# Kernel optimization log

Measured on AMD Instinct MI355X. Metric: run time of the kernel, lower is better.

The kernel has to match this reference:

```python
import jax, jax.numpy as jnp
import numpy as np

N = 4096
D = 256
H = 8
HD = D // H
EPS = 1e-5
NEG = -1e9


def layer_norm(x, g, b):
    mu = jnp.mean(x, axis=-1, keepdims=True)
    var = jnp.mean(jnp.square(x - mu), axis=-1, keepdims=True)
    return (x - mu) * jax.lax.rsqrt(var + EPS) * g + b


def setup_inputs() -> dict:
    key = jax.random.key(0)
    ks = jax.random.split(key, 12)
    s = 1.0 / np.sqrt(D)
    inp = {
        "x": jax.random.normal(ks[0], (N, D), dtype=jnp.float32),
        "adj": jax.random.randint(ks[1], (N, N), 0, 2, dtype=jnp.int32),
        "Wq": jax.random.uniform(ks[2], (D, D), jnp.float32, -s, s),
        "Wk": jax.random.uniform(ks[3], (D, D), jnp.float32, -s, s),
        "Wv": jax.random.uniform(ks[4], (D, D), jnp.float32, -s, s),
        "bq": jnp.zeros((D,), jnp.float32),
        "bk": jnp.zeros((D,), jnp.float32),
        "bv": jnp.zeros((D,), jnp.float32),
        "Wo": jax.random.uniform(ks[5], (D, D), jnp.float32, -s, s),
        "bo": jnp.zeros((D,), jnp.float32),
        "g1": jnp.ones((D,), jnp.float32),
        "beta1": jnp.zeros((D,), jnp.float32),
        "W1": jax.random.uniform(ks[6], (2 * D, D), jnp.float32, -s, s),
        "b1": jnp.zeros((2 * D,), jnp.float32),
        "W2": jax.random.uniform(ks[7], (D, 2 * D), jnp.float32, -1.0 / np.sqrt(2 * D), 1.0 / np.sqrt(2 * D)),
        "b2": jnp.zeros((D,), jnp.float32),
        "g2": jnp.ones((D,), jnp.float32),
        "beta2": jnp.zeros((D,), jnp.float32),
    }
    return inp


def reference(x, adj, Wq, Wk, Wv, bq, bk, bv, Wo, bo, g1, beta1, W1, b1, W2, b2, g2, beta2):
    n = adj.shape[0]
    # allowed = adj + I > 0 ; attention only over neighbors + self-loop
    allowed = (adj + jnp.eye(n, dtype=adj.dtype)) > 0  # (n, n) bool

    q = (x @ Wq.T + bq).reshape(n, H, HD)
    k = (x @ Wk.T + bk).reshape(n, H, HD)
    v = (x @ Wv.T + bv).reshape(n, H, HD)

    scale = 1.0 / np.sqrt(HD)
    scores = jnp.einsum('nhd,mhd->hnm', q, k) * scale  # (H, n, n)
    scores = jnp.where(allowed[None, :, :], scores, NEG)
    attn = jax.nn.softmax(scores, axis=-1)
    o = jnp.einsum('hnm,mhd->nhd', attn, v).reshape(n, D)
    h = o @ Wo.T + bo

    x = layer_norm(x + h, g1, beta1)
    ffn = jax.nn.relu(x @ W1.T + b1) @ W2.T + b2
    x = layer_norm(x + ffn, g2, beta2)
    return x
```

## Files before the change

kernel.cpp:

```cpp
#include <hip/hip_runtime.h>
#include <hip/hip_bf16.h>

typedef __attribute__((ext_vector_type(4))) float f32x4;
typedef __attribute__((ext_vector_type(8))) short s16x8;

#define NROWS 4096
#define DMODEL 256
#define NHEAD 8
#define HDIM 32
#define PSTRIDE 72
#define OSTRIDE 33
#define M2C 24.0f
#define NM (NROWS * DMODEL)
#define SH_S 268
#define SY_S 264
#define SR_S 520

__device__ __forceinline__ short bf16r(float f) {
    union { float f; unsigned u; } v; v.f = f;
    unsigned r = v.u + 0x7fffu + ((v.u >> 16) & 1u);
    return (short)(r >> 16);
}

__device__ __forceinline__ float fexp2(float x) {
    float r;
    asm("v_exp_f32 %0, %1" : "=v"(r) : "v"(x));
    return r;
}

__device__ __forceinline__ unsigned pk_bf16(float a, float b) {
#if __has_builtin(__builtin_amdgcn_cvt_pk_bf16_f32)
    typedef __bf16 bf2 __attribute__((ext_vector_type(2)));
    union { bf2 h; unsigned u; } c;
    c.h = __builtin_amdgcn_cvt_pk_bf16_f32(a, b);
    return c.u;
#else
    return (unsigned)(unsigned short)bf16r(a) | ((unsigned)(unsigned short)bf16r(b) << 16);
#endif
}

__device__ __forceinline__ s16x8 pack8(float4 a, float4 b) {
    s16x8 r;
    r[0] = bf16r(a.x); r[1] = bf16r(a.y); r[2] = bf16r(a.z); r[3] = bf16r(a.w);
    r[4] = bf16r(b.x); r[5] = bf16r(b.y); r[6] = bf16r(b.z); r[7] = bf16r(b.w);
    return r;
}

__global__ __launch_bounds__(256) void qkvprep_kernel(
        const float* __restrict__ X,
        const float* __restrict__ Wq, const float* __restrict__ Wk,
        const float* __restrict__ Wv,
        const float* __restrict__ bq, const float* __restrict__ bk,
        const float* __restrict__ bv,
        const int* __restrict__ adj, unsigned* __restrict__ mask,
        const float* __restrict__ Wo, const float* __restrict__ W1,
        const float* __restrict__ W2, short* __restrict__ Wb,
        short* __restrict__ Qb, short* __restrict__ Kb,
        short* __restrict__ Vswz) {
    __shared__ short sT[64 * 72];
    const int b = blockIdx.x;
    const int tid = threadIdx.x;
    const int lane = tid & 63;
    if (b < 768) {
        const int wv = tid >> 6;
        const int quad = lane >> 4, col = lane & 15;
        const int bx = b & 63, by = b >> 6;
        const int o0 = by * 64;
        const int z = o0 >> 8;
        const float* Wsrc = (z == 0) ? Wq : (z == 1 ? Wk : Wv);
        const float* bias = (z == 0) ? bq : (z == 1 ? bk : bv);
        const int ow0 = o0 & 255;
        const int n0 = bx * 64 + wv * 16;
        const float QSC = 0.25505653437397888f;

        f32x4 zero = {0.f, 0.f, 0.f, 0.f};
        f32x4 acc[4] = {zero, zero, zero, zero};
        const float* ap = X + (size_t)(n0 + col) * DMODEL + quad * 8;
#pragma unroll
        for (int k0 = 0; k0 < DMODEL; k0 += 32) {
            float4 a0 = *(const float4*)(ap + k0);
            float4 a1 = *(const float4*)(ap + k0 + 4);
            s16x8 af = pack8(a0, a1);
#pragma unroll
            for (int t = 0; t < 4; ++t) {
                const float* wp = Wsrc + (size_t)(ow0 + t * 16 + col) * DMODEL + quad * 8 + k0;
                s16x8 bf = pack8(*(const float4*)wp, *(const float4*)(wp + 4));
                acc[t] = __builtin_amdgcn_mfma_f32_16x16x32_bf16(af, bf, acc[t], 0, 0, 0);
            }
        }
        if (z != 2) {
#pragma unroll
            for (int t = 0; t < 4; ++t) {
                const int oo = ow0 + t * 16 + col;
                float bvv = bias[oo];
#pragma unroll
                for (int r = 0; r < 4; ++r) {
                    int n = n0 + quad * 4 + r;
                    float v = acc[t][r] + bvv;
                    if (z == 0) Qb[(size_t)n * DMODEL + oo] = bf16r(v * QSC);
                    else        Kb[(size_t)(oo >> 5) * NROWS * HDIM + (size_t)n * HDIM + (oo & 31)] = bf16r(v);
                }
            }
        } else {
#pragma unroll
            for (int t = 0; t < 4; ++t) {
                const int oot = t * 16 + col;
                float bvv = bias[ow0 + oot];
#pragma unroll
                for (int r = 0; r < 4; ++r) {
                    int nn = wv * 16 + quad * 4 + r;
                    sT[oot * 72 + nn] = bf16r(acc[t][r] + bvv);
                }
            }
            __syncthreads();
            const int f = tid >> 5;
            const int lh = f >> 2, hdh = (f >> 1) & 1, kh = f & 1;
            const int L0 = (tid & 31) * 2;
            const int hgl = (ow0 >> 5) + lh;
            short* dst = Vswz + (((size_t)(hgl * 64 + bx) * 4 + hdh * 2 + kh) * 512);
#pragma unroll
            for (int e = 0; e < 2; ++e) {
                int L = L0 + e;
                int hd_local = lh * 32 + hdh * 16 + (L & 15);
                int key_local = kh * 32 + ((L >> 4) * 8);
                s16x8 v = *(const s16x8*)&sT[hd_local * 72 + key_local];
                *(s16x8*)(dst + L * 8) = v;
            }
        }
    } else if (b < 2816) {
        const int waveid = (b - 768) * 4 + (tid >> 6);
        int4 av[8];
        int rows[8], segs[8];
#pragma unroll
        for (int i = 0; i < 8; ++i) {
            const int task = waveid + i * 8192;
            rows[i] = task >> 4; segs[i] = task & 15;
            av[i] = *(const int4*)(adj + (size_t)rows[i] * NROWS + segs[i] * 256 + lane * 4);
        }
#pragma unroll
        for (int i = 0; i < 8; ++i) {
            const int row = rows[i];
            const int c0 = segs[i] * 256 + lane * 4;
            unsigned nib = (unsigned)(av[i].x > 0 || c0 == row)
                         | ((unsigned)(av[i].y > 0 || c0 + 1 == row) << 1)
                         | ((unsigned)(av[i].z > 0 || c0 + 2 == row) << 2)
                         | ((unsigned)(av[i].w > 0 || c0 + 3 == row) << 3);
            unsigned v = nib << ((lane & 7) * 4);
            v |= __shfl_xor((int)v, 1, 64);
            v |= __shfl_xor((int)v, 2, 64);
            v |= __shfl_xor((int)v, 4, 64);
            if ((lane & 7) == 0)
                mask[row * 128 + segs[i] * 8 + (lane >> 3)] = v;
        }
    } else {
        int i = (b - 2816) * 2048 + tid * 8;
        const float* src; int off;
        if (i < 65536)       { src = Wo; off = i; }
        else if (i < 196608) { src = W1; off = i - 65536; }
        else                 { src = W2; off = i - 196608; }
        float4 a = *(const float4*)(src + off);
        float4 c = *(const float4*)(src + off + 4);
        *(s16x8*)(Wb + i) = pack8(a, c);
    }
}

__global__ __launch_bounds__(256) void attn_kernel(const short* __restrict__ Qb,
                                                   const short* __restrict__ Kb,
                                                   const short* __restrict__ Vswz,
                                                   const unsigned* __restrict__ mask,
                                                   short* __restrict__ Om) {
    __shared__ union {
        short sP[2][16 * PSTRIDE];
        float sO[HDIM][OSTRIDE];
    } u[4];
    __shared__ float sl[4][32];

    const int tid = threadIdx.x;
    const int wv = tid >> 6, lane = tid & 63;
    const int quad = lane >> 4, col = lane & 15;
    const int h = blockIdx.x & 7;
    const int q0 = (blockIdx.x >> 3) * 32;
    const int kw = wv * 1024;

    s16x8 qf[2];
    qf[0] = *(const s16x8*)(Qb + (size_t)(q0 + col) * DMODEL + h * HDIM + quad * 8);
    qf[1] = *(const s16x8*)(Qb + (size_t)(q0 + 16 + col) * DMODEL + h * HDIM + quad * 8);

    const short* kp = Kb + (size_t)h * NROWS * HDIM + (size_t)(kw + col) * HDIM + quad * 8;
    const short* vbase = Vswz + ((size_t)(h * 64 + (kw >> 6)) * 4) * 512 + lane * 8;
    const unsigned* mp0 = mask + (size_t)(q0 + col) * 128 + (kw >> 5);
    const unsigned* mp1 = mp0 + 16 * 128;

    const short onev = (col == 0) ? (short)0x3F80 : (short)0;
    const s16x8 ones = {onev, onev, onev, onev, onev, onev, onev, onev};

    f32x4 zero = {0.f, 0.f, 0.f, 0.f};
    f32x4 acc[2][2] = {{zero, zero}, {zero, zero}};
    f32x4 lacc[2] = {zero, zero};
    const f32x4 cinit = {-M2C, -M2C, -M2C, -M2C};

#pragma unroll 2
    for (int it = 0; it < 16; ++it) {
        const short* k = kp + it * 64 * HDIM;
        s16x8 kf0 = *(const s16x8*)(k);
        s16x8 kf1 = *(const s16x8*)(k + 16 * HDIM);
        s16x8 kf2 = *(const s16x8*)(k + 32 * HDIM);
        s16x8 kf3 = *(const s16x8*)(k + 48 * HDIM);
        uint2 w0 = *(const uint2*)(mp0 + it * 2);
        uint2 w1 = *(const uint2*)(mp1 + it * 2);
        const short* vb = vbase + it * 4 * 512;
        s16x8 vf00 = *(const s16x8*)(vb);
        s16x8 vf01 = *(const s16x8*)(vb + 512);
        s16x8 vf10 = *(const s16x8*)(vb + 1024);
        s16x8 vf11 = *(const s16x8*)(vb + 1536);

#pragma unroll
        for (int qs = 0; qs < 2; ++qs) {
            unsigned wlo = (qs ? w1.x : w0.x) >> (quad * 4);
            unsigned whi = (qs ? w1.y : w0.y) >> (quad * 4);
            f32x4 st[4];
            st[0] = __builtin_amdgcn_mfma_f32_16x16x32_bf16(kf0, qf[qs], cinit, 0, 0, 0);
            st[1] = __builtin_amdgcn_mfma_f32_16x16x32_bf16(kf1, qf[qs], cinit, 0, 0, 0);
            st[2] = __builtin_amdgcn_mfma_f32_16x16x32_bf16(kf2, qf[qs], cinit, 0, 0, 0);
            st[3] = __builtin_amdgcn_mfma_f32_16x16x32_bf16(kf3, qf[qs], cinit, 0, 0, 0);

            float p[4][4];
#pragma unroll
            for (int t = 0; t < 4; ++t) {
                unsigned wm = (t < 2) ? wlo : whi;
#pragma unroll
                for (int r = 0; r < 4; ++r) {
                    float e = fexp2(st[t][r]);
                    bool ok = (wm & (1u << ((t & 1) * 16 + r))) != 0u;
                    p[t][r] = ok ? e : 0.f;
                }
            }

            short* pb = &u[wv].sP[qs][0];
#pragma unroll
            for (int t = 0; t < 4; ++t) {
                uint2 pr;
                pr.x = pk_bf16(p[t][0], p[t][1]);
                pr.y = pk_bf16(p[t][2], p[t][3]);
                *(uint2*)(pb + col * PSTRIDE + t * 16 + quad * 4) = pr;
            }
            s16x8 pb0 = *(const s16x8*)(pb + col * PSTRIDE + quad * 8);
            s16x8 pb1 = *(const s16x8*)(pb + col * PSTRIDE + 32 + quad * 8);

            acc[qs][0] = __builtin_amdgcn_mfma_f32_16x16x32_bf16(vf00, pb0, acc[qs][0], 0, 0, 0);
            acc[qs][0] = __builtin_amdgcn_mfma_f32_16x16x32_bf16(vf01, pb1, acc[qs][0], 0, 0, 0);
            acc[qs][1] = __builtin_amdgcn_mfma_f32_16x16x32_bf16(vf10, pb0, acc[qs][1], 0, 0, 0);
            acc[qs][1] = __builtin_amdgcn_mfma_f32_16x16x32_bf16(vf11, pb1, acc[qs][1], 0, 0, 0);
            lacc[qs] = __builtin_amdgcn_mfma_f32_16x16x32_bf16(ones, pb0, lacc[qs], 0, 0, 0);
            lacc[qs] = __builtin_amdgcn_mfma_f32_16x16x32_bf16(ones, pb1, lacc[qs], 0, 0, 0);
        }
    }

#pragma unroll
    for (int qs = 0; qs < 2; ++qs) {
        if (lane < 16) sl[wv][qs * 16 + col] = lacc[qs][0];
#pragma unroll
        for (int rr = 0; rr < 4; ++rr) {
            u[wv].sO[quad * 4 + rr][qs * 16 + col]      = acc[qs][0][rr];
            u[wv].sO[16 + quad * 4 + rr][qs * 16 + col] = acc[qs][1][rr];
        }
    }
    __syncthreads();

    const int q = tid >> 3, hd0 = (tid & 7) * 4;
    float l = sl[0][q] + sl[1][q] + sl[2][q] + sl[3][q];
    float inv = 1.f / l;
    float4 ov;
    ov.x = u[0].sO[hd0][q]     + u[1].sO[hd0][q]     + u[2].sO[hd0][q]     + u[3].sO[hd0][q];
    ov.y = u[0].sO[hd0 + 1][q] + u[1].sO[hd0 + 1][q] + u[2].sO[hd0 + 1][q] + u[3].sO[hd0 + 1][q];
    ov.z = u[0].sO[hd0 + 2][q] + u[1].sO[hd0 + 2][q] + u[2].sO[hd0 + 2][q] + u[3].sO[hd0 + 2][q];
    ov.w = u[0].sO[hd0 + 3][q] + u[1].sO[hd0 + 3][q] + u[2].sO[hd0 + 3][q] + u[3].sO[hd0 + 3][q];
    uint2 ob;
    ob.x = pk_bf16(ov.x * inv, ov.y * inv);
    ob.y = pk_bf16(ov.z * inv, ov.w * inv);
    *(uint2*)(Om + (size_t)(q0 + q) * DMODEL + h * HDIM + hd0) = ob;
}

__global__ __launch_bounds__(512) void mega_kernel(
        const short* __restrict__ Omb,
        const float* __restrict__ X,
        const short* __restrict__ Wob, const short* __restrict__ W1b,
        const short* __restrict__ W2b,
        const float* __restrict__ bo,
        const float* __restrict__ g1, const float* __restrict__ be1,
        const float* __restrict__ b1, const float* __restrict__ b2,
        const float* __restrict__ g2, const float* __restrict__ be2,
        float* __restrict__ out) {
    __shared__ short sR[16 * SR_S];
    __shared__ float sH[16 * SH_S];
    __shared__ short sY[16 * SY_S];

    const int tid = threadIdx.x;
    const int wv = tid >> 6, lane = tid & 63;
    const int quad = lane >> 4, col = lane & 15;
    const int n0 = blockIdx.x * 16;
    const int rr_ = tid >> 5, c8 = (tid & 31) * 8;
    const int n_ln = n0 + rr_;
    f32x4 zero = {0.f, 0.f, 0.f, 0.f};

    {
        const int o0 = wv * 32;
        f32x4 acc[2] = {zero, zero};
#pragma unroll
        for (int k0 = 0; k0 < DMODEL; k0 += 32) {
            s16x8 af = *(const s16x8*)(Omb + (size_t)(n0 + col) * DMODEL + k0 + quad * 8);
#pragma unroll
            for (int t = 0; t < 2; ++t) {
                s16x8 bf = *(const s16x8*)(Wob + (size_t)(o0 + t * 16 + col) * DMODEL + k0 + quad * 8);
                acc[t] = __builtin_amdgcn_mfma_f32_16x16x32_bf16(af, bf, acc[t], 0, 0, 0);
            }
        }
#pragma unroll
        for (int t = 0; t < 2; ++t) {
            int o = o0 + t * 16 + col;
            float bv = bo[o];
#pragma unroll
            for (int r = 0; r < 4; ++r)
                sH[(quad * 4 + r) * SH_S + o] = acc[t][r] + bv;
        }
    }
    __syncthreads();

    float y1v[8];
    {
        const float* xp = X + (size_t)n_ln * DMODEL + c8;
        float v[8];
        float s = 0.f;
#pragma unroll
        for (int j = 0; j < 2; ++j) {
            float4 xv = ((const float4*)xp)[j];
            float4 hv = *(const float4*)&sH[rr_ * SH_S + c8 + j * 4];
            v[j * 4 + 0] = xv.x + hv.x; v[j * 4 + 1] = xv.y + hv.y;
            v[j * 4 + 2] = xv.z + hv.z; v[j * 4 + 3] = xv.w + hv.w;
            s += v[j * 4] + v[j * 4 + 1] + v[j * 4 + 2] + v[j * 4 + 3];
        }
#pragma unroll
        for (int m = 1; m < 32; m <<= 1) s += __shfl_xor(s, m, 64);
        float mean = s * (1.f / 256.f);
        float q = 0.f;
#pragma unroll
        for (int i = 0; i < 8; ++i) { v[i] -= mean; q += v[i] * v[i]; }
#pragma unroll
        for (int m = 1; m < 32; m <<= 1) q += __shfl_xor(q, m, 64);
        float rstd = rsqrtf(q * (1.f / 256.f) + 1e-5f);
        const float* gp = g1 + c8;
        const float* bp = be1 + c8;
        s16x8 w;
#pragma unroll
        for (int j = 0; j < 2; ++j) {
            float4 gv = ((const float4*)gp)[j];
            float4 bev = ((const float4*)bp)[j];
            float a0 = v[j * 4 + 0] * rstd * gv.x + bev.x;
            float a1 = v[j * 4 + 1] * rstd * gv.y + bev.y;
            float a2 = v[j * 4 + 2] * rstd * gv.z + bev.z;
            float a3 = v[j * 4 + 3] * rstd * gv.w + bev.w;
            y1v[j * 4 + 0] = a0; y1v[j * 4 + 1] = a1;
            y1v[j * 4 + 2] = a2; y1v[j * 4 + 3] = a3;
            *((unsigned*)&w + j * 2 + 0) = pk_bf16(a0, a1);
            *((unsigned*)&w + j * 2 + 1) = pk_bf16(a2, a3);
        }
        *(s16x8*)&sY[rr_ * SY_S + c8] = w;
    }
    __syncthreads();

    {
        const int o0 = wv * 64;
        f32x4 acc[4] = {zero, zero, zero, zero};
#pragma unroll
        for (int k0 = 0; k0 < DMODEL; k0 += 32) {
            s16x8 af = *(const s16x8*)&sY[col * SY_S + k0 + quad * 8];
#pragma unroll
            for (int t = 0; t < 4; ++t) {
                s16x8 bf = *(const s16x8*)(W1b + (size_t)(o0 + t * 16 + col) * DMODEL + k0 + quad * 8);
                acc[t] = __builtin_amdgcn_mfma_f32_16x16x32_bf16(af, bf, acc[t], 0, 0, 0);
            }
        }
#pragma unroll
        for (int t = 0; t < 4; ++t) {
            int o = o0 + t * 16 + col;
            float bv = b1[o];
#pragma unroll
            for (int r = 0; r < 4; ++r)
                sR[(quad * 4 + r) * SR_S + o] = bf16r(fmaxf(acc[t][r] + bv, 0.f));
        }
    }
    __syncthreads();

    {
        const int o0 = wv * 32;
        f32x4 acc[2] = {zero, zero};
#pragma unroll
        for (int k0 = 0; k0 < 512; k0 += 32) {
            s16x8 af = *(const s16x8*)&sR[col * SR_S + k0 + quad * 8];
#pragma unroll
            for (int t = 0; t < 2; ++t) {
                s16x8 bf = *(const s16x8*)(W2b + (size_t)(o0 + t * 16 + col) * 512 + k0 + quad * 8);
                acc[t] = __builtin_amdgcn_mfma_f32_16x16x32_bf16(af, bf, acc[t], 0, 0, 0);
            }
        }
#pragma unroll
        for (int t = 0; t < 2; ++t) {
            int o = o0 + t * 16 + col;
            float bv = b2[o];
#pragma unroll
            for (int r = 0; r < 4; ++r)
                sH[(quad * 4 + r) * SH_S + o] = acc[t][r] + bv;
        }
    }
    __syncthreads();

    {
        float v[8];
        float s = 0.f;
#pragma unroll
        for (int j = 0; j < 2; ++j) {
            float4 hv = *(const float4*)&sH[rr_ * SH_S + c8 + j * 4];
            v[j * 4 + 0] = y1v[j * 4 + 0] + hv.x; v[j * 4 + 1] = y1v[j * 4 + 1] + hv.y;
            v[j * 4 + 2] = y1v[j * 4 + 2] + hv.z; v[j * 4 + 3] = y1v[j * 4 + 3] + hv.w;
            s += v[j * 4] + v[j * 4 + 1] + v[j * 4 + 2] + v[j * 4 + 3];
        }
#pragma unroll
        for (int m = 1; m < 32; m <<= 1) s += __shfl_xor(s, m, 64);
        float mean = s * (1.f / 256.f);
        float q = 0.f;
#pragma unroll
        for (int i = 0; i < 8; ++i) { v[i] -= mean; q += v[i] * v[i]; }
#pragma unroll
        for (int m = 1; m < 32; m <<= 1) q += __shfl_xor(q, m, 64);
        float rstd = rsqrtf(q * (1.f / 256.f) + 1e-5f);
        const float* gp = g2 + c8;
        const float* bp = be2 + c8;
        float* op = out + (size_t)n_ln * DMODEL + c8;
#pragma unroll
        for (int j = 0; j < 2; ++j) {
            float4 gv = ((const float4*)gp)[j];
            float4 bev = ((const float4*)bp)[j];
            float4 y;
            y.x = v[j * 4 + 0] * rstd * gv.x + bev.x;
            y.y = v[j * 4 + 1] * rstd * gv.y + bev.y;
            y.z = v[j * 4 + 2] * rstd * gv.z + bev.z;
            y.w = v[j * 4 + 3] * rstd * gv.w + bev.w;
            ((float4*)op)[j] = y;
        }
    }
}

extern "C" void kernel_launch(void* const* d_in, const int* in_sizes, int n_in,
                              void* d_out, int out_size, void* d_ws, size_t ws_size,
                              hipStream_t stream) {
    const float* x   = (const float*)d_in[0];
    const int*   adj = (const int*)d_in[1];
    const float* Wq  = (const float*)d_in[2];
    const float* Wk  = (const float*)d_in[3];
    const float* Wv  = (const float*)d_in[4];
    const float* bq  = (const float*)d_in[5];
    const float* bk  = (const float*)d_in[6];
    const float* bv  = (const float*)d_in[7];
    const float* Wo  = (const float*)d_in[8];
    const float* bo  = (const float*)d_in[9];
    const float* g1  = (const float*)d_in[10];
    const float* be1 = (const float*)d_in[11];
    const float* W1  = (const float*)d_in[12];
    const float* b1  = (const float*)d_in[13];
    const float* W2  = (const float*)d_in[14];
    const float* b2  = (const float*)d_in[15];
    const float* g2  = (const float*)d_in[16];
    const float* be2 = (const float*)d_in[17];
    float* out = (float*)d_out;

    char* p = (char*)d_ws;
    unsigned* mask = (unsigned*)p; p += (size_t)NROWS * 128 * 4;
    short* Wb   = (short*)p;       p += (size_t)327680 * 2;
    short* Qb   = (short*)p;       p += (size_t)NM * 2;
    short* Kb   = (short*)p;       p += (size_t)NM * 2;
    short* Vswz = (short*)p;       p += (size_t)NM * 2;
    short* Omb  = (short*)p;       p += (size_t)NM * 2;

    qkvprep_kernel<<<dim3(2976), dim3(256), 0, stream>>>(
        x, Wq, Wk, Wv, bq, bk, bv, adj, mask, Wo, W1, W2, Wb, Qb, Kb, Vswz);
    attn_kernel<<<dim3(1024), dim3(256), 0, stream>>>(Qb, Kb, Vswz, mask, Omb);
    mega_kernel<<<dim3(256), dim3(512), 0, stream>>>(
        Omb, x, Wb, Wb + 65536, Wb + 196608,
        bo, g1, be1, b1, b2, g2, be2, out);
}
```

Measured before the change: 224.8 us.

## Pre-convert X and QKV weights to bf16 in a separate kernel; LUT-based mask in attention

The fused prep kernel is split in two. The first kernel builds the adjacency bitmask and converts Wo/W1/W2, Wq/Wk/Wv and X to bf16. The second runs the QKV projection from those bf16 buffers, so the GEMM no longer repacks fp32 to bf16 on every load. The attention inner loop now applies the mask by ANDing packed bf16 exp values with 16-bit masks fetched from a small shared-memory lookup table, replacing the per-element select. The split adds a kernel launch and an extra global round trip for X, and the table adds LDS reads per tile.

```diff
diff --git a/kernel.cpp b/kernel.cpp
--- a/kernel.cpp
+++ b/kernel.cpp
@@ -46,89 +46,18 @@
     return r;
 }
 
-__global__ __launch_bounds__(256) void qkvprep_kernel(
-        const float* __restrict__ X,
-        const float* __restrict__ Wq, const float* __restrict__ Wk,
-        const float* __restrict__ Wv,
-        const float* __restrict__ bq, const float* __restrict__ bk,
-        const float* __restrict__ bv,
+__global__ __launch_bounds__(256) void prep1_kernel(
         const int* __restrict__ adj, unsigned* __restrict__ mask,
         const float* __restrict__ Wo, const float* __restrict__ W1,
         const float* __restrict__ W2, short* __restrict__ Wb,
-        short* __restrict__ Qb, short* __restrict__ Kb,
-        short* __restrict__ Vswz) {
-    __shared__ short sT[64 * 72];
+        const float* __restrict__ Wq, const float* __restrict__ Wk,
+        const float* __restrict__ Wv, short* __restrict__ Wqkvb,
+        const float* __restrict__ X, short* __restrict__ Xb) {
     const int b = blockIdx.x;
     const int tid = threadIdx.x;
     const int lane = tid & 63;
-    if (b < 768) {
-        const int wv = tid >> 6;
-        const int quad = lane >> 4, col = lane & 15;
-        const int bx = b & 63, by = b >> 6;
-        const int o0 = by * 64;
-        const int z = o0 >> 8;
-        const float* Wsrc = (z == 0) ? Wq : (z == 1 ? Wk : Wv);
-        const float* bias = (z == 0) ? bq : (z == 1 ? bk : bv);
-        const int ow0 = o0 & 255;
-        const int n0 = bx * 64 + wv * 16;
-        const float QSC = 0.25505653437397888f;
-
-        f32x4 zero = {0.f, 0.f, 0.f, 0.f};
-        f32x4 acc[4] = {zero, zero, zero, zero};
-        const float* ap = X + (size_t)(n0 + col) * DMODEL + quad * 8;
-#pragma unroll
-        for (int k0 = 0; k0 < DMODEL; k0 += 32) {
-            float4 a0 = *(const float4*)(ap + k0);
-            float4 a1 = *(const float4*)(ap + k0 + 4);
-            s16x8 af = pack8(a0, a1);
-#pragma unroll
-            for (int t = 0; t < 4; ++t) {
-                const float* wp = Wsrc + (size_t)(ow0 + t * 16 + col) * DMODEL + quad * 8 + k0;
-                s16x8 bf = pack8(*(const float4*)wp, *(const float4*)(wp + 4));
-                acc[t] = __builtin_amdgcn_mfma_f32_16x16x32_bf16(af, bf, acc[t], 0, 0, 0);
-            }
-        }
-        if (z != 2) {
-#pragma unroll
-            for (int t = 0; t < 4; ++t) {
-                const int oo = ow0 + t * 16 + col;
-                float bvv = bias[oo];
-#pragma unroll
-                for (int r = 0; r < 4; ++r) {
-                    int n = n0 + quad * 4 + r;
-                    float v = acc[t][r] + bvv;
-                    if (z == 0) Qb[(size_t)n * DMODEL + oo] = bf16r(v * QSC);
-                    else        Kb[(size_t)(oo >> 5) * NROWS * HDIM + (size_t)n * HDIM + (oo & 31)] = bf16r(v);
-                }
-            }
-        } else {
-#pragma unroll
-            for (int t = 0; t < 4; ++t) {
-                const int oot = t * 16 + col;
-                float bvv = bias[ow0 + oot];
-#pragma unroll
-                for (int r = 0; r < 4; ++r) {
-                    int nn = wv * 16 + quad * 4 + r;
-                    sT[oot * 72 + nn] = bf16r(acc[t][r] + bvv);
-                }
-            }
-            __syncthreads();
-            const int f = tid >> 5;
-            const int lh = f >> 2, hdh = (f >> 1) & 1, kh = f & 1;
-            const int L0 = (tid & 31) * 2;
-            const int hgl = (ow0 >> 5) + lh;
-            short* dst = Vswz + (((size_t)(hgl * 64 + bx) * 4 + hdh * 2 + kh) * 512);
-#pragma unroll
-            for (int e = 0; e < 2; ++e) {
-                int L = L0 + e;
-                int hd_local = lh * 32 + hdh * 16 + (L & 15);
-                int key_local = kh * 32 + ((L >> 4) * 8);
-                s16x8 v = *(const s16x8*)&sT[hd_local * 72 + key_local];
-                *(s16x8*)(dst + L * 8) = v;
-            }
-        }
-    } else if (b < 2816) {
-        const int waveid = (b - 768) * 4 + (tid >> 6);
+    if (b < 2048) {
+        const int waveid = b * 4 + (tid >> 6);
         int4 av[8];
         int rows[8], segs[8];
 #pragma unroll
@@ -152,15 +81,96 @@
             if ((lane & 7) == 0)
                 mask[row * 128 + segs[i] * 8 + (lane >> 3)] = v;
         }
-    } else {
-        int i = (b - 2816) * 2048 + tid * 8;
+    } else if (b < 2208) {
+        int i = (b - 2048) * 2048 + tid * 8;
         const float* src; int off;
         if (i < 65536)       { src = Wo; off = i; }
         else if (i < 196608) { src = W1; off = i - 65536; }
         else                 { src = W2; off = i - 196608; }
-        float4 a = *(const float4*)(src + off);
-        float4 c = *(const float4*)(src + off + 4);
-        *(s16x8*)(Wb + i) = pack8(a, c);
+        *(s16x8*)(Wb + i) = pack8(*(const float4*)(src + off), *(const float4*)(src + off + 4));
+    } else if (b < 2304) {
+        int i = (b - 2208) * 2048 + tid * 8;
+        const float* src; int off;
+        if (i < 65536)       { src = Wq; off = i; }
+        else if (i < 131072) { src = Wk; off = i - 65536; }
+        else                 { src = Wv; off = i - 131072; }
+        *(s16x8*)(Wqkvb + i) = pack8(*(const float4*)(src + off), *(const float4*)(src + off + 4));
+    } else {
+        int i = (b - 2304) * 2048 + tid * 8;
+        *(s16x8*)(Xb + i) = pack8(*(const float4*)(X + i), *(const float4*)(X + i + 4));
+    }
+}
+
+__global__ __launch_bounds__(256) void prep2_kernel(
+        const short* __restrict__ Xb, const short* __restrict__ Wqkvb,
+        const float* __restrict__ bq, const float* __restrict__ bk,
+        const float* __restrict__ bv,
+        short* __restrict__ Qb, short* __restrict__ Kb,
+        short* __restrict__ Vswz) {
+    __shared__ short sT[64 * 72];
+    const int b = blockIdx.x;
+    const int tid = threadIdx.x;
+    const int lane = tid & 63;
+    const int wv = tid >> 6;
+    const int quad = lane >> 4, col = lane & 15;
+    const int bx = b & 63, by = b >> 6;
+    const int o0 = by * 64;
+    const int z = o0 >> 8;
+    const float* bias = (z == 0) ? bq : (z == 1 ? bk : bv);
+    const int ow0 = o0 & 255;
+    const int n0 = bx * 64 + wv * 16;
+    const float QSC = 0.25505653437397888f;
+
+    f32x4 zero = {0.f, 0.f, 0.f, 0.f};
+    f32x4 acc[4] = {zero, zero, zero, zero};
+    const short* ap = Xb + (size_t)(n0 + col) * DMODEL + quad * 8;
+#pragma unroll
+    for (int k0 = 0; k0 < DMODEL; k0 += 32) {
+        s16x8 af = *(const s16x8*)(ap + k0);
+#pragma unroll
+        for (int t = 0; t < 4; ++t) {
+            s16x8 bf = *(const s16x8*)(Wqkvb + (size_t)(o0 + t * 16 + col) * DMODEL + quad * 8 + k0);
+            acc[t] = __builtin_amdgcn_mfma_f32_16x16x32_bf16(af, bf, acc[t], 0, 0, 0);
+        }
+    }
+    if (z != 2) {
+#pragma unroll
+        for (int t = 0; t < 4; ++t) {
+            const int oo = ow0 + t * 16 + col;
+            float bvv = bias[oo];
+#pragma unroll
+            for (int r = 0; r < 4; ++r) {
+                int n = n0 + quad * 4 + r;
+                float v = acc[t][r] + bvv;
+                if (z == 0) Qb[(size_t)n * DMODEL + oo] = bf16r(v * QSC);
+                else        Kb[(size_t)(oo >> 5) * NROWS * HDIM + (size_t)n * HDIM + (oo & 31)] = bf16r(v);
+            }
+        }
+    } else {
+#pragma unroll
+        for (int t = 0; t < 4; ++t) {
+            const int oot = t * 16 + col;
+            float bvv = bias[ow0 + oot];
+#pragma unroll
+            for (int r = 0; r < 4; ++r) {
+                int nn = wv * 16 + quad * 4 + r;
+                sT[oot * 72 + nn] = bf16r(acc[t][r] + bvv);
+            }
+        }
+        __syncthreads();
+        const int f = tid >> 5;
+        const int lh = f >> 2, hdh = (f >> 1) & 1, kh = f & 1;
+        const int L0 = (tid & 31) * 2;
+        const int hgl = (ow0 >> 5) + lh;
+        short* dst = Vswz + (((size_t)(hgl * 64 + bx) * 4 + hdh * 2 + kh) * 512);
+#pragma unroll
+        for (int e = 0; e < 2; ++e) {
+            int L = L0 + e;
+            int hd_local = lh * 32 + hdh * 16 + (L & 15);
+            int key_local = kh * 32 + ((L >> 4) * 8);
+            s16x8 v = *(const s16x8*)&sT[hd_local * 72 + key_local];
+            *(s16x8*)(dst + L * 8) = v;
+        }
     }
 }
 
@@ -174,6 +184,7 @@
         float sO[HDIM][OSTRIDE];
     } u[4];
     __shared__ float sl[4][32];
+    __shared__ __align__(16) unsigned lut2[32];
 
     const int tid = threadIdx.x;
     const int wv = tid >> 6, lane = tid & 63;
@@ -182,6 +193,14 @@
     const int q0 = (blockIdx.x >> 3) * 32;
     const int kw = wv * 1024;
 
+    if (tid < 32) {
+        int i = tid >> 1;
+        unsigned b0 = (tid & 1) ? ((i >> 2) & 1u) : (i & 1u);
+        unsigned b1 = (tid & 1) ? ((i >> 3) & 1u) : ((i >> 1) & 1u);
+        lut2[tid] = (b0 ? 0xFFFFu : 0u) | (b1 ? 0xFFFF0000u : 0u);
+    }
+    __syncthreads();
+
     s16x8 qf[2];
     qf[0] = *(const s16x8*)(Qb + (size_t)(q0 + col) * DMODEL + h * HDIM + quad * 8);
     qf[1] = *(const s16x8*)(Qb + (size_t)(q0 + 16 + col) * DMODEL + h * HDIM + quad * 8);
@@ -198,6 +217,8 @@
     f32x4 acc[2][2] = {{zero, zero}, {zero, zero}};
     f32x4 lacc[2] = {zero, zero};
     const f32x4 cinit = {-M2C, -M2C, -M2C, -M2C};
+    const int sh_lo = quad * 4, sh_hi = 16 + quad * 4;
+    const char* lb = (const char*)lut2;
 
 #pragma unroll 2
     for (int it = 0; it < 16; ++it) {
@@ -216,34 +237,34 @@
 
 #pragma unroll
         for (int qs = 0; qs < 2; ++qs) {
-            unsigned wlo = (qs ? w1.x : w0.x) >> (quad * 4);
-            unsigned whi = (qs ? w1.y : w0.y) >> (quad * 4);
+            const unsigned wx = qs ? w1.x : w0.x;
+            const unsigned wy = qs ? w1.y : w0.y;
+            uint2 m0 = *(const uint2*)(lb + (((wx >> sh_lo) & 0xF) << 3));
+            uint2 m1 = *(const uint2*)(lb + (((wx >> sh_hi) & 0xF) << 3));
+            uint2 m2 = *(const uint2*)(lb + (((wy >> sh_lo) & 0xF) << 3));
+            uint2 m3 = *(const uint2*)(lb + (((wy >> sh_hi) & 0xF) << 3));
+
             f32x4 st[4];
             st[0] = __builtin_amdgcn_mfma_f32_16x16x32_bf16(kf0, qf[qs], cinit, 0, 0, 0);
             st[1] = __builtin_amdgcn_mfma_f32_16x16x32_bf16(kf1, qf[qs], cinit, 0, 0, 0);
             st[2] = __builtin_amdgcn_mfma_f32_16x16x32_bf16(kf2, qf[qs], cinit, 0, 0, 0);
             st[3] = __builtin_amdgcn_mfma_f32_16x16x32_bf16(kf3, qf[qs], cinit, 0, 0, 0);
 
-            float p[4][4];
-#pragma unroll
-            for (int t = 0; t < 4; ++t) {
-                unsigned wm = (t < 2) ? wlo : whi;
-#pragma unroll
-                for (int r = 0; r < 4; ++r) {
-                    float e = fexp2(st[t][r]);
-                    bool ok = (wm & (1u << ((t & 1) * 16 + r))) != 0u;
-                    p[t][r] = ok ? e : 0.f;
-                }
-            }
-
             short* pb = &u[wv].sP[qs][0];
-#pragma unroll
-            for (int t = 0; t < 4; ++t) {
-                uint2 pr;
-                pr.x = pk_bf16(p[t][0], p[t][1]);
-                pr.y = pk_bf16(p[t][2], p[t][3]);
-                *(uint2*)(pb + col * PSTRIDE + t * 16 + quad * 4) = pr;
-            }
+            uint2 pr;
+            pr.x = pk_bf16(fexp2(st[0][0]), fexp2(st[0][1])) & m0.x;
+            pr.y = pk_bf16(fexp2(st[0][2]), fexp2(st[0][3])) & m0.y;
+            *(uint2*)(pb + col * PSTRIDE + 0 * 16 + quad * 4) = pr;
+            pr.x = pk_bf16(fexp2(st[1][0]), fexp2(st[1][1])) & m1.x;
+            pr.y = pk_bf16(fexp2(st[1][2]), fexp2(st[1][3])) & m1.y;
+            *(uint2*)(pb + col * PSTRIDE + 1 * 16 + quad * 4) = pr;
+            pr.x = pk_bf16(fexp2(st[2][0]), fexp2(st[2][1])) & m2.x;
+            pr.y = pk_bf16(fexp2(st[2][2]), fexp2(st[2][3])) & m2.y;
+            *(uint2*)(pb + col * PSTRIDE + 2 * 16 + quad * 4) = pr;
+            pr.x = pk_bf16(fexp2(st[3][0]), fexp2(st[3][1])) & m3.x;
+            pr.y = pk_bf16(fexp2(st[3][2]), fexp2(st[3][3])) & m3.y;
+            *(uint2*)(pb + col * PSTRIDE + 3 * 16 + quad * 4) = pr;
+
             s16x8 pb0 = *(const s16x8*)(pb + col * PSTRIDE + quad * 8);
             s16x8 pb1 = *(const s16x8*)(pb + col * PSTRIDE + 32 + quad * 8);
 
@@ -475,14 +496,18 @@
 
     char* p = (char*)d_ws;
     unsigned* mask = (unsigned*)p; p += (size_t)NROWS * 128 * 4;
-    short* Wb   = (short*)p;       p += (size_t)327680 * 2;
-    short* Qb   = (short*)p;       p += (size_t)NM * 2;
-    short* Kb   = (short*)p;       p += (size_t)NM * 2;
-    short* Vswz = (short*)p;       p += (size_t)NM * 2;
-    short* Omb  = (short*)p;       p += (size_t)NM * 2;
-
-    qkvprep_kernel<<<dim3(2976), dim3(256), 0, stream>>>(
-        x, Wq, Wk, Wv, bq, bk, bv, adj, mask, Wo, W1, W2, Wb, Qb, Kb, Vswz);
+    short* Wb    = (short*)p;      p += (size_t)327680 * 2;
+    short* Wqkvb = (short*)p;      p += (size_t)196608 * 2;
+    short* Xb    = (short*)p;      p += (size_t)NM * 2;
+    short* Qb    = (short*)p;      p += (size_t)NM * 2;
+    short* Kb    = (short*)p;      p += (size_t)NM * 2;
+    short* Vswz  = (short*)p;      p += (size_t)NM * 2;
+    short* Omb   = (short*)p;      p += (size_t)NM * 2;
+
+    prep1_kernel<<<dim3(2816), dim3(256), 0, stream>>>(
+        adj, mask, Wo, W1, W2, Wb, Wq, Wk, Wv, Wqkvb, x, Xb);
+    prep2_kernel<<<dim3(768), dim3(256), 0, stream>>>(
+        Xb, Wqkvb, bq, bk, bv, Qb, Kb, Vswz);
     attn_kernel<<<dim3(1024), dim3(256), 0, stream>>>(Qb, Kb, Vswz, mask, Omb);
     mega_kernel<<<dim3(256), dim3(512), 0, stream>>>(
         Omb, x, Wb, Wb + 65536, Wb + 196608,
```

Result: faster. 212.2 us (-5.6%).
